# Optimization experiments

Hardware: AMD Instinct MI355X
Metric: run time of the kernel (lower is better)

Reference implementation:

```python
import jax, jax.numpy as jnp
import numpy as np

B, T, N, D = 8, 32, 24, 128          # batch, seq_len, max_node_num, roi_feature_size
H_LINK, H_LSTM, C, P = 128, 128, 6, 3  # link hidden, lstm hidden, big_attr_classes, propagate_layers


def setup_inputs() -> dict:
    key = jax.random.key(0)
    ks = jax.random.split(key, 20)
    node_num_rec = jax.random.randint(ks[0], (B, T), 2, N + 1)  # valid nodes per frame
    node_mask = jnp.arange(N)[None, None, :] < node_num_rec[:, :, None]          # [B,T,N]
    pair_mask = node_mask[:, :, :, None] & node_mask[:, :, None, :]              # [B,T,N,N]
    offdiag = ~jnp.eye(N, dtype=bool)
    # post-ResNet ROI features; invalid nodes / self-edges are zero (as in the torch code)
    node_resnet = jax.random.normal(ks[1], (B, T, D, N)) * node_mask[:, :, None, :]
    edge_resnet = jax.random.normal(ks[2], (B, T, D, N, N)) * (pair_mask & offdiag)[:, :, None]

    def w(k, shape, fan):
        return jax.random.normal(k, shape) / np.sqrt(fan)

    return dict(
        node_resnet=node_resnet, edge_resnet=edge_resnet,
        link_W1=w(ks[3], (H_LINK, D), D), link_b1=jnp.zeros((H_LINK,)),
        link_W2=w(ks[4], (1, H_LINK), H_LINK), link_b2=jnp.zeros((1,)),
        msg_Wh=w(ks[5], (D, D), 2 * D), msg_We=w(ks[6], (D, D), 2 * D), msg_b=jnp.zeros((D,)),
        gru_Wih=w(ks[7], (3 * D, D), D), gru_Whh=w(ks[8], (3 * D, D), D),
        gru_bih=jnp.zeros((3 * D,)), gru_bhh=jnp.zeros((3 * D,)),
        lstm_Wih=w(ks[9], (4 * H_LSTM, D), D), lstm_Whh=w(ks[10], (4 * H_LSTM, H_LSTM), H_LSTM),
        lstm_bih=jnp.zeros((4 * H_LSTM,)), lstm_bhh=jnp.zeros((4 * H_LSTM,)),
        ro_W=w(ks[11], (C, H_LSTM), H_LSTM), ro_b=jnp.zeros((C,)),
        node_num_rec=node_num_rec,
    )


def reference(node_resnet, edge_resnet, link_W1, link_b1, link_W2, link_b2,
              msg_Wh, msg_We, msg_b, gru_Wih, gru_Whh, gru_bih, gru_bhh,
              lstm_Wih, lstm_Whh, lstm_bih, lstm_bhh, ro_W, ro_b, node_num_rec):
    node_mask = jnp.arange(N)[None, None, :] < node_num_rec[:, :, None]      # [B,T,N]
    pair_mask = node_mask[:, :, :, None] & node_mask[:, :, None, :]          # [B,T,N,N]
    fmask_n = node_mask[:, :, None, :].astype(node_resnet.dtype)             # [B,T,1,N]
    fmask_p = pair_mask.astype(node_resnet.dtype)                            # [B,T,N,N]

    h_node = node_resnet      # [B,T,D,N]
    h_edge = edge_resnet      # [B,T,D,N,N]
    for _ in range(P):
        # link_fun (GraphConv = per-edge 1x1-conv MLP) -> adjacency logits, sigmoid gate on valid pairs
        hid = jax.nn.relu(jnp.einsum('btdvw,hd->bthvw', h_edge, link_W1)
                          + link_b1[None, None, :, None, None])
        adj = jnp.einsum('bthvw,h->btvw', hid, link_W2[0]) + link_b2[0]      # [B,T,N,N]
        gate = jax.nn.sigmoid(adj) * fmask_p
        # message_fun 'linear_concat_relu': relu(W @ concat(h_w, e_vw) + b), e_vw is raw edge feature
        msg = jax.nn.relu(jnp.einsum('btdw,od->btow', h_node, msg_Wh)[:, :, :, None, :]
                          + jnp.einsum('btdvw,od->btovw', edge_resnet, msg_We)
                          + msg_b[None, None, :, None, None])                # [B,T,D,N,N]
        gated = gate[:, :, None] * msg
        # hidden edge states of next round: gated messages in valid region, clone of edge feats elsewhere
        h_edge = jnp.where(pair_mask[:, :, None], gated, edge_resnet)
        m_v = jnp.sum(gated, axis=-1)                                        # [B,T,D,N] sum over senders
        # update_fun: single-step GRU, input m_v, hidden h_node
        x = m_v.transpose(0, 1, 3, 2)      # [B,T,N,D]
        h = h_node.transpose(0, 1, 3, 2)
        gi = x @ gru_Wih.T + gru_bih
        gh = h @ gru_Whh.T + gru_bhh
        i_r, i_z, i_n = jnp.split(gi, 3, axis=-1)
        h_r, h_z, h_n = jnp.split(gh, 3, axis=-1)
        r = jax.nn.sigmoid(i_r + h_r)
        z = jax.nn.sigmoid(i_z + h_z)
        n = jnp.tanh(i_n + r * h_n)
        h_new = ((1.0 - z) * n + z * h).transpose(0, 1, 3, 2)                # [B,T,D,N]
        h_node = jnp.where(node_mask[:, :, None, :], h_new, node_resnet)

    # temporal LSTM over seq dim; node (and batch) axis acts as LSTM batch, zero initial state
    x_seq = h_node.transpose(1, 0, 3, 2).reshape(T, B * N, D)
    h0 = jnp.zeros((B * N, H_LSTM), dtype=x_seq.dtype)
    c0 = jnp.zeros_like(h0)

    def cell(carry, xt):
        h, c = carry
        g = xt @ lstm_Wih.T + lstm_bih + h @ lstm_Whh.T + lstm_bhh
        i, f, gg, o = jnp.split(g, 4, axis=-1)
        c = jax.nn.sigmoid(f) * c + jax.nn.sigmoid(i) * jnp.tanh(gg)
        h = jax.nn.sigmoid(o) * jnp.tanh(c)
        return (h, c), h

    _, out = jax.lax.scan(cell, (h0, c0), x_seq)                             # [T,B*N,H]
    out = out.reshape(T, B, N, H_LSTM).transpose(1, 0, 2, 3)                 # [B,T,N,H]
    pred_label = (out @ ro_W.T + ro_b) * node_mask[..., None]                # [B,T,N,C]
    return pred_label
```

## Files before the change

kernel.cpp:

```cpp
#include <hip/hip_runtime.h>
#include <cmath>

typedef unsigned short u16;
typedef unsigned int   u32;
typedef short bf16x8 __attribute__((ext_vector_type(8)));
typedef float f32x4 __attribute__((ext_vector_type(4)));

constexpr int B_ = 8, T_ = 32, N_ = 24, D_ = 128;
constexpr int BT_ = B_ * T_;
constexpr int VW_ = N_ * N_;
constexpr int BTN_ = BT_ * N_;
constexpr int BTVW_ = BT_ * VW_;
constexpr int P_ = 3;
constexpr int C_ = 6;
constexpr int SA_ = 136;

__device__ __forceinline__ float bits2f(u32 u) { float f; __builtin_memcpy(&f, &u, 4); return f; }
__device__ __forceinline__ float bf2f(u16 h) { return bits2f(((u32)h) << 16); }
__device__ __forceinline__ u16 f2bf(float f) {
    u32 u; __builtin_memcpy(&u, &f, 4);
    u32 r = u + 0x7FFFu + ((u >> 16) & 1u);
    return (u16)(r >> 16);
}
__device__ __forceinline__ f32x4 ld4bf(const u16* p) {
    const uint2 v = *(const uint2*)p;
    f32x4 r;
    r[0] = bf2f((u16)v.x); r[1] = bf2f((u16)(v.x >> 16));
    r[2] = bf2f((u16)v.y); r[3] = bf2f((u16)(v.y >> 16));
    return r;
}
__device__ __forceinline__ float fexp2(float x) { return __builtin_amdgcn_exp2f(x); }
__device__ __forceinline__ float frcp(float x) { return __builtin_amdgcn_rcpf(x); }
__device__ __forceinline__ float sigm(float x) {
    return frcp(1.0f + fexp2(x * -1.4426950408889634f));
}
__device__ __forceinline__ float ftanh(float x) {
    const float t = fexp2(fabsf(x) * -2.8853900817779268f);
    return copysignf((1.0f - t) * frcp(1.0f + t), x);
}

struct PreArgs {
    const float* node; float* HN; u16* HNb;
    const float* fsrc[7]; u16* fdst[7]; int fstart[8];
    const void* csrc[10]; u16* cdst[10]; int cstart[11];
};

__global__ __launch_bounds__(256) void k_preproc(PreArgs a) {
    const int bx = blockIdx.x;
    if (bx < 256) {
        const int bt = bx;
        for (int f = threadIdx.x; f < 3072; f += 256) {
            const int d = f / 24, n = f - d * 24;
            const float v = a.node[(size_t)bt * 3072 + f];
            a.HN[(size_t)bt * 3072 + n * 128 + d] = v;
            a.HNb[(size_t)bt * 3072 + n * 128 + d] = f2bf(v);
        }
    } else if (bx < 1344) {
        const int idx = (bx - 256) * 256 + threadIdx.x;
        if (idx >= a.fstart[7]) return;
        int s = 0;
#pragma unroll
        for (int i = 1; i < 7; ++i) s += (idx >= a.fstart[i]) ? 1 : 0;
        const int off = idx - a.fstart[s];
        const int e = off & 7, lane = (off >> 3) & 63;
        const int ks = (off >> 9) & 3, rb = off >> 11;
        const int m = lane & 15, quad = lane >> 4;
        a.fdst[s][off] = f2bf(a.fsrc[s][(size_t)(rb * 16 + m) * 128 + ks * 32 + quad * 8 + e]);
    } else {
        const int idx = (bx - 1344) * 256 + threadIdx.x;
        if (idx >= a.cstart[10]) return;
        int s = 0;
#pragma unroll
        for (int i = 1; i < 10; ++i) s += (idx >= a.cstart[i]) ? 1 : 0;
        const int off = idx - a.cstart[s];
        a.cdst[s][off] = f2bf(((const float*)a.csrc[s])[off]);
    }
}

__global__ __launch_bounds__(64) void k_prep(
    const float* __restrict__ edge, const u16* __restrict__ WeF,
    const u16* __restrict__ W1F, const u16* __restrict__ b1,
    const u16* __restrict__ W2, const u16* __restrict__ b2,
    u16* __restrict__ ME, float* __restrict__ ADJ) {
    __shared__ __align__(16) u16 A[32 * 128];
    const int tid = threadIdx.x;
    const int bt = blockIdx.x / 18, tile = blockIdx.x % 18;
    const int vw0 = tile * 32;
    const size_t ebase = (size_t)bt * D_ * VW_ + vw0;
    const int vq = tid & 7, dg = tid >> 3;
    u32* A32 = (u32*)A;
#pragma unroll
    for (int batch = 0; batch < 2; ++batch) {
        float4 fa[4], fb[4];
#pragma unroll
        for (int j = 0; j < 4; ++j) {
            const int it = batch * 4 + j;
            const int d0 = it * 16 + dg * 2;
            fa[j] = *(const float4*)&edge[ebase + (size_t)d0 * VW_ + vq * 4];
            fb[j] = *(const float4*)&edge[ebase + (size_t)(d0 + 1) * VW_ + vq * 4];
        }
#pragma unroll
        for (int j = 0; j < 4; ++j) {
            const int it = batch * 4 + j;
            const int d0 = it * 16 + dg * 2;
            const float* pa = (const float*)&fa[j];
            const float* pb = (const float*)&fb[j];
#pragma unroll
            for (int i = 0; i < 4; ++i) {
                const int row = vq * 4 + i;
                const int sw32 = ((row >> 2) & 7) * 4;
                A32[row * 64 + ((d0 >> 1) ^ sw32)] =
                    (u32)f2bf(pa[i]) | ((u32)f2bf(pb[i]) << 16);
            }
        }
    }
    __syncthreads();
    const int m = tid & 15, quad = tid >> 4;
    bf16x8 a[2][4];
#pragma unroll
    for (int rt = 0; rt < 2; ++rt) {
        const int row = rt * 16 + m;
        const int sw16 = ((row >> 2) & 7) * 8;
#pragma unroll
        for (int ks = 0; ks < 4; ++ks)
            a[rt][ks] = *(const bf16x8*)&A[row * 128 + ((ks * 32 + quad * 8) ^ sw16)];
    }
    const f32x4 z = {0.f, 0.f, 0.f, 0.f};
#pragma unroll
    for (int ct = 0; ct < 8; ++ct) {
        bf16x8 bw[4];
#pragma unroll
        for (int ks = 0; ks < 4; ++ks)
            bw[ks] = *(const bf16x8*)&WeF[((ct * 4 + ks) << 9) + tid * 8];
        f32x4 acc[2];
#pragma unroll
        for (int rt = 0; rt < 2; ++rt) acc[rt] = z;
#pragma unroll
        for (int rt = 0; rt < 2; ++rt)
#pragma unroll
            for (int ks = 0; ks < 4; ++ks)
                acc[rt] = __builtin_amdgcn_mfma_f32_16x16x32_bf16(bw[ks], a[rt][ks], acc[rt], 0, 0, 0);
#pragma unroll
        for (int rt = 0; rt < 2; ++rt) {
            const u32 lo = (u32)f2bf(acc[rt][0]) | ((u32)f2bf(acc[rt][1]) << 16);
            const u32 hi = (u32)f2bf(acc[rt][2]) | ((u32)f2bf(acc[rt][3]) << 16);
            *(uint2*)&ME[(size_t)(bt * VW_ + vw0 + rt * 16 + m) * 128 + ct * 16 + quad * 4] =
                make_uint2(lo, hi);
        }
    }
    float p[2][4] = {};
    const float b2v = bf2f(b2[0]);
#pragma unroll
    for (int ct = 0; ct < 8; ++ct) {
        bf16x8 bw[4];
#pragma unroll
        for (int ks = 0; ks < 4; ++ks)
            bw[ks] = *(const bf16x8*)&W1F[((ct * 4 + ks) << 9) + tid * 8];
        f32x4 acc[2];
#pragma unroll
        for (int rt = 0; rt < 2; ++rt) acc[rt] = z;
#pragma unroll
        for (int rt = 0; rt < 2; ++rt)
#pragma unroll
            for (int ks = 0; ks < 4; ++ks)
                acc[rt] = __builtin_amdgcn_mfma_f32_16x16x32_bf16(a[rt][ks], bw[ks], acc[rt], 0, 0, 0);
        const int n = ct * 16 + m;
        const float b1v = bf2f(b1[n]);
        const float w2v = bf2f(W2[n]);
#pragma unroll
        for (int rt = 0; rt < 2; ++rt)
#pragma unroll
            for (int reg = 0; reg < 4; ++reg)
                p[rt][reg] += fmaxf(acc[rt][reg] + b1v, 0.0f) * w2v;
    }
#pragma unroll
    for (int rt = 0; rt < 2; ++rt)
#pragma unroll
        for (int reg = 0; reg < 4; ++reg) {
            float v = p[rt][reg];
            v += __shfl_xor(v, 1);
            v += __shfl_xor(v, 2);
            v += __shfl_xor(v, 4);
            v += __shfl_xor(v, 8);
            p[rt][reg] = v;
        }
    if (m == 0) {
#pragma unroll
        for (int rt = 0; rt < 2; ++rt)
#pragma unroll
            for (int reg = 0; reg < 4; ++reg)
                ADJ[bt * VW_ + vw0 + rt * 16 + quad * 4 + reg] = p[rt][reg] + b2v;
    }
}

template <bool ADJP>
__global__ __launch_bounds__(256) void k_fused(
    const u16* __restrict__ ME, const float* __restrict__ XW,
    const u16* __restrict__ mb,
    const u16* __restrict__ W1F, const u16* __restrict__ b1,
    const u16* __restrict__ W2, const u16* __restrict__ b2,
    const int* __restrict__ nnr, float* __restrict__ ADJ,
    u16* __restrict__ MVb) {
    __shared__ __align__(16) u16 A[48 * SA_];
    __shared__ float gate_s[48];
    __shared__ float2 mvp[2][2][64];
    const int tid = threadIdx.x;
    const int blk = blockIdx.x;
    const int bt = blk / 12, pr = blk - bt * 12;
    const int v0 = pr * 2;
    const int e0 = bt * VW_ + v0 * N_;
    const int nv = nnr[bt];

    if (tid < 48) gate_s[tid] = sigm(ADJ[e0 + tid]);
    __syncthreads();
    {
        const int op = tid & 63;
        const int sub = (tid >> 6) & 1;
        const int grp = tid >> 7;
        const int v = v0 + grp;
        const u32 mbu = ((const u32*)mb)[op];
        const float mb0 = bf2f((u16)mbu), mb1 = bf2f((u16)(mbu >> 16));
        const bool vva = v < nv;
        u32 meR[12]; float2 xwR[12];
#pragma unroll
        for (int i = 0; i < 12; ++i) {
            const int w = sub * 12 + i;
            const int rr = grp * 24 + w;
            meR[i] = ((const u32*)ME)[(size_t)(e0 + rr) * 64 + op];
            xwR[i] = *(const float2*)&XW[(size_t)(bt * N_ + w) * 128 + 2 * op];
        }
        float mvx = 0.0f, mvy = 0.0f;
        u32* A32 = (u32*)A;
#pragma unroll
        for (int i = 0; i < 12; ++i) {
            const int w = sub * 12 + i;
            const int rr = grp * 24 + w;
            float v0f = 0.0f, v1f = 0.0f;
            if (vva && w < nv) {
                const float g = gate_s[rr];
                v0f = g * fmaxf(xwR[i].x + bf2f((u16)meR[i]) + mb0, 0.0f);
                v1f = g * fmaxf(xwR[i].y + bf2f((u16)(meR[i] >> 16)) + mb1, 0.0f);
                mvx += v0f; mvy += v1f;
            }
            if (ADJP) A32[rr * 68 + op] = (u32)f2bf(v0f) | ((u32)f2bf(v1f) << 16);
        }
        mvp[grp][sub][op] = make_float2(mvx, mvy);
    }
    __syncthreads();
    if (tid < 128) {
        const int g2 = tid >> 6, o2 = tid & 63;
        const float2 pa = mvp[g2][0][o2], pb = mvp[g2][1][o2];
        ((u32*)MVb)[(size_t)(bt * N_ + v0 + g2) * 64 + o2] =
            (u32)f2bf(pa.x + pb.x) | ((u32)f2bf(pa.y + pb.y) << 16);
    }

    if constexpr (ADJP) {
        __syncthreads();
        if (tid >= 64) return;
        const int m = tid & 15, quad = tid >> 4;
        bf16x8 a[3][4];
#pragma unroll
        for (int rt = 0; rt < 3; ++rt)
#pragma unroll
            for (int ks = 0; ks < 4; ++ks)
                a[rt][ks] = *(const bf16x8*)&A[(rt * 16 + m) * SA_ + ks * 32 + quad * 8];
        const f32x4 z = {0.f, 0.f, 0.f, 0.f};
        float p[3][4] = {};
        const float b2v = bf2f(b2[0]);
#pragma unroll
        for (int ct = 0; ct < 8; ++ct) {
            bf16x8 bw[4];
#pragma unroll
            for (int ks = 0; ks < 4; ++ks)
                bw[ks] = *(const bf16x8*)&W1F[((ct * 4 + ks) << 9) + tid * 8];
            f32x4 acc[3];
#pragma unroll
            for (int rt = 0; rt < 3; ++rt) acc[rt] = z;
#pragma unroll
            for (int rt = 0; rt < 3; ++rt)
#pragma unroll
                for (int ks = 0; ks < 4; ++ks)
                    acc[rt] = __builtin_amdgcn_mfma_f32_16x16x32_bf16(a[rt][ks], bw[ks], acc[rt], 0, 0, 0);
            const int n = ct * 16 + m;
            const float b1v = bf2f(b1[n]);
            const float w2v = bf2f(W2[n]);
#pragma unroll
            for (int rt = 0; rt < 3; ++rt)
#pragma unroll
                for (int reg = 0; reg < 4; ++reg)
                    p[rt][reg] += fmaxf(acc[rt][reg] + b1v, 0.0f) * w2v;
        }
#pragma unroll
        for (int rt = 0; rt < 3; ++rt)
#pragma unroll
            for (int reg = 0; reg < 4; ++reg) {
                float v = p[rt][reg];
                v += __shfl_xor(v, 1);
                v += __shfl_xor(v, 2);
                v += __shfl_xor(v, 4);
                v += __shfl_xor(v, 8);
                p[rt][reg] = v;
            }
        if (m == 0) {
#pragma unroll
            for (int rt = 0; rt < 3; ++rt)
#pragma unroll
                for (int reg = 0; reg < 4; ++reg)
                    ADJ[e0 + rt * 16 + quad * 4 + reg] = p[rt][reg] + b2v;
        }
    }
}

__global__ __launch_bounds__(64, 1) void k_xw(const u16* __restrict__ HNb,
                                              const u16* __restrict__ WhF,
                                              float* __restrict__ XW) {
    const int tid = threadIdx.x;
    const int m = tid & 15, quad = tid >> 4;
    const int r0 = blockIdx.x * 16;
    const int ct0 = blockIdx.y * 2;
    bf16x8 a[4];
#pragma unroll
    for (int ks = 0; ks < 4; ++ks)
        a[ks] = *(const bf16x8*)&HNb[(size_t)(r0 + m) * 128 + ks * 32 + quad * 8];
    const f32x4 z = {0.f, 0.f, 0.f, 0.f};
#pragma unroll
    for (int cti = 0; cti < 2; ++cti) {
        const int ct = ct0 + cti;
        f32x4 acc = z;
#pragma unroll
        for (int ks = 0; ks < 4; ++ks) {
            const bf16x8 b = *(const bf16x8*)&WhF[((ct * 4 + ks) << 9) + tid * 8];
            acc = __builtin_amdgcn_mfma_f32_16x16x32_bf16(b, a[ks], acc, 0, 0, 0);
        }
        *(f32x4*)&XW[(size_t)(r0 + m) * 128 + ct * 16 + quad * 4] = acc;
    }
}

__global__ __launch_bounds__(64, 1) void k_gruM(
    const u16* __restrict__ MVb, const u16* __restrict__ HNb_in,
    float* __restrict__ HN, u16* __restrict__ HNb,
    const u16* __restrict__ WihF, const u16* __restrict__ WhhF,
    const u16* __restrict__ bih, const u16* __restrict__ bhh,
    const int* __restrict__ nnr) {
    const int tid = threadIdx.x;
    const int m = tid & 15, quad = tid >> 4;
    const int rbase = blockIdx.x * 16;
    const int ct0 = blockIdx.y * 2;
    bf16x8 amv[4], ahn[4];
#pragma unroll
    for (int ks = 0; ks < 4; ++ks) {
        amv[ks] = *(const bf16x8*)&MVb[(size_t)(rbase + m) * 128 + ks * 32 + quad * 8];
        ahn[ks] = *(const bf16x8*)&HNb_in[(size_t)(rbase + m) * 128 + ks * 32 + quad * 8];
    }
    const int myrow = rbase + m;
    const int mybt = myrow / N_;
    const bool valid = (myrow - mybt * N_) < nnr[mybt];
    const f32x4 z = {0.f, 0.f, 0.f, 0.f};
#pragma unroll
    for (int cti = 0; cti < 2; ++cti) {
        const int ct = ct0 + cti;
        f32x4 gi[3], gh[3];
#pragma unroll
        for (int g = 0; g < 3; ++g) { gi[g] = z; gh[g] = z; }
#pragma unroll
        for (int g = 0; g < 3; ++g) {
            const int rb = g * 8 + ct;
#pragma unroll
            for (int ks = 0; ks < 4; ++ks) {
                const bf16x8 bi_f = *(const bf16x8*)&WihF[((rb * 4 + ks) << 9) + tid * 8];
                const bf16x8 bh_f = *(const bf16x8*)&WhhF[((rb * 4 + ks) << 9) + tid * 8];
                gi[g] = __builtin_amdgcn_mfma_f32_16x16x32_bf16(bi_f, amv[ks], gi[g], 0, 0, 0);
                gh[g] = __builtin_amdgcn_mfma_f32_16x16x32_bf16(bh_f, ahn[ks], gh[g], 0, 0, 0);
            }
        }
        const int col0 = ct * 16 + quad * 4;
        const f32x4 biR = ld4bf(&bih[col0]),       bhR = ld4bf(&bhh[col0]);
        const f32x4 biZ = ld4bf(&bih[128 + col0]), bhZ = ld4bf(&bhh[128 + col0]);
        const f32x4 biN = ld4bf(&bih[256 + col0]), bhN = ld4bf(&bhh[256 + col0]);
        const size_t oi = (size_t)myrow * 128 + col0;
        const f32x4 hold = *(const f32x4*)&HN[oi];
        f32x4 hv;
#pragma unroll
        for (int reg = 0; reg < 4; ++reg) {
            const float r  = sigm(gi[0][reg] + gh[0][reg] + biR[reg] + bhR[reg]);
            const float zz = sigm(gi[1][reg] + gh[1][reg] + biZ[reg] + bhZ[reg]);
            const float nn = ftanh(gi[2][reg] + biN[reg] + r * (gh[2][reg] + bhN[reg]));
            hv[reg] = valid ? ((1.0f - zz) * nn + zz * hold[reg]) : 0.0f;
        }
        *(f32x4*)&HN[oi] = hv;
        const u32 lo = (u32)f2bf(hv[0]) | ((u32)f2bf(hv[1]) << 16);
        const u32 hi = (u32)f2bf(hv[2]) | ((u32)f2bf(hv[3]) << 16);
        *(uint2*)&HNb[oi] = make_uint2(lo, hi);
    }
}

__global__ __launch_bounds__(64, 2) void k_gi(const u16* __restrict__ HNb,
                                              const u16* __restrict__ WF,
                                              const u16* __restrict__ bih, const u16* __restrict__ bhh,
                                              float* __restrict__ GI2) {
    const int tid = threadIdx.x;
    const int m = tid & 15, quad = tid >> 4;
    const int r0 = blockIdx.x * 16;
    const int ocol0 = blockIdx.y * 64;
    const int r = r0 + m;
    const int btq = r / 24, n = r - btq * 24;
    const int b = btq >> 5, t = btq & 31;
    const int q = b * 24 + n;
    const int blk = q >> 4, mrow = q & 15;
    bf16x8 a[4];
#pragma unroll
    for (int ks = 0; ks < 4; ++ks)
        a[ks] = *(const bf16x8*)&HNb[(size_t)r * 128 + ks * 32 + quad * 8];
    const f32x4 z = {0.f, 0.f, 0.f, 0.f};
#pragma unroll
    for (int ct = 0; ct < 4; ++ct) {
        f32x4 acc = z;
        const int rb = blockIdx.y * 4 + ct;
#pragma unroll
        for (int ks = 0; ks < 4; ++ks) {
            const bf16x8 bb = *(const bf16x8*)&WF[((rb * 4 + ks) << 9) + tid * 8];
            acc = __builtin_amdgcn_mfma_f32_16x16x32_bf16(bb, a[ks], acc, 0, 0, 0);
        }
        const int col0 = ocol0 + ct * 16 + quad * 4;
        const f32x4 bi4 = ld4bf(&bih[col0]);
        const f32x4 bh4 = ld4bf(&bhh[col0]);
#pragma unroll
        for (int reg = 0; reg < 4; ++reg) acc[reg] += bi4[reg] + bh4[reg];
        const int cta = (ocol0 >> 4) + ct;
        const int w = cta & 7, j = cta >> 3;
        const size_t addr = ((size_t)(blk * 32 + t) * 512 + (w * 64 + quad * 16 + mrow)) * 16 + j * 4;
        *(f32x4*)&GI2[addr] = acc;
    }
}

__global__ __launch_bounds__(512) void k_rec(const float* __restrict__ GI2,
                                             const u16* __restrict__ WhhF,
                                             float* __restrict__ OUTH) {
    __shared__ __align__(16) u16 Abuf[2][16 * 128];
    const int tid = threadIdx.x;
    const int w = tid >> 6, lane = tid & 63;
    const int m = lane & 15, quad = lane >> 4;
    const int blk = blockIdx.x;
    const int q = blk * 16 + m;
    bf16x8 bw[4][4];
#pragma unroll
    for (int j = 0; j < 4; ++j)
#pragma unroll
        for (int ks = 0; ks < 4; ++ks)
            bw[j][ks] = *(const bf16x8*)&WhhF[(((j * 8 + w) * 4 + ks) << 9) + lane * 8];
    const f32x4 z = {0.f, 0.f, 0.f, 0.f};
    f32x4 cst = z;
    bf16x8 a[4];
#pragma unroll
    for (int ks = 0; ks < 4; ++ks) a[ks] = (bf16x8)(short)0;
    const float* gb = GI2 + ((size_t)blk * 32 * 512 + tid) * 16;
    f32x4 g[4], gn[4];
#pragma unroll
    for (int j = 0; j < 4; ++j) g[j] = *(const f32x4*)&gb[j * 4];
    const int ws = w * 2 + (quad >> 1);
    const int woff = (quad & 1) * 2;
    for (int t = 0; t < T_; ++t) {
        const int tn = (t + 1 < T_) ? (t + 1) : (T_ - 1);
        const size_t gnb = (size_t)tn * 512 * 16;
#pragma unroll
        for (int j = 0; j < 4; ++j) gn[j] = *(const f32x4*)&gb[gnb + j * 4];
        f32x4 acc[4];
#pragma unroll
        for (int j = 0; j < 4; ++j) acc[j] = z;
#pragma unroll
        for (int j = 0; j < 4; ++j)
#pragma unroll
            for (int ks = 0; ks < 4; ++ks)
                acc[j] = __builtin_amdgcn_mfma_f32_16x16x32_bf16(bw[j][ks], a[ks], acc[j], 0, 0, 0);
        f32x4 hv;
#pragma unroll
        for (int r = 0; r < 4; ++r) {
            const float gi_ = acc[0][r] + g[0][r];
            const float gf_ = acc[1][r] + g[1][r];
            const float gg_ = acc[2][r] + g[2][r];
            const float go_ = acc[3][r] + g[3][r];
            cst[r] = sigm(gf_) * cst[r] + sigm(gi_) * ftanh(gg_);
            hv[r] = sigm(go_) * ftanh(cst[r]);
        }
        *(f32x4*)&OUTH[((size_t)t * 192 + q) * 128 + w * 16 + quad * 4] = hv;
        const u32 lo = (u32)f2bf(hv[0]) | ((u32)f2bf(hv[1]) << 16);
        const u32 hi = (u32)f2bf(hv[2]) | ((u32)f2bf(hv[3]) << 16);
        u32* dst = (u32*)&Abuf[(t + 1) & 1][0];
        *(uint2*)&dst[m * 64 + ((ws ^ m) << 2) + woff] = make_uint2(lo, hi);
        __syncthreads();
        const u16* src = &Abuf[(t + 1) & 1][0];
#pragma unroll
        for (int ks = 0; ks < 4; ++ks)
            a[ks] = *(const bf16x8*)&src[m * 128 + (((ks * 4 + quad) ^ m) << 3)];
#pragma unroll
        for (int j = 0; j < 4; ++j) g[j] = gn[j];
    }
}

__global__ __launch_bounds__(256) void k_readout(const float* __restrict__ OUTH,
                                                 const u16* __restrict__ roW,
                                                 const u16* __restrict__ rob,
                                                 const int* __restrict__ nnr,
                                                 float* __restrict__ out) {
    const int idx = blockIdx.x * 256 + threadIdx.x;
    const int btn = idx / C_, c = idx - btn * C_;
    const int bt = btn / N_, n = btn - bt * N_;
    const int b = bt / T_, t = bt - b * T_;
    const int nv = nnr[bt];
    float val = 0.0f;
    if (n < nv) {
        const float* hrow = OUTH + ((size_t)t * 192 + b * N_ + n) * 128;
        const uint2* w2 = (const uint2*)&roW[c * 128];
        float acc = bf2f(rob[c]);
#pragma unroll
        for (int k4 = 0; k4 < 32; ++k4) {
            const float4 h4 = *(const float4*)&hrow[k4 * 4];
            const uint2 ww = w2[k4];
            acc = fmaf(bf2f((u16)ww.x), h4.x,
                  fmaf(bf2f((u16)(ww.x >> 16)), h4.y,
                  fmaf(bf2f((u16)ww.y), h4.z,
                  fmaf(bf2f((u16)(ww.y >> 16)), h4.w, acc))));
        }
        val = acc;
    }
    out[idx] = val;
}

extern "C" void kernel_launch(void* const* d_in, const int* in_sizes, int n_in,
                              void* d_out, int out_size, void* d_ws, size_t ws_size,
                              hipStream_t stream) {
    const float* node = (const float*)d_in[0];
    const float* edge = (const float*)d_in[1];
    const int* nnr = (const int*)d_in[19];

    char* ws = (char*)d_ws;
    float* HN = (float*)ws;   ws += (size_t)BTN_ * D_ * 4;
    u16* HNb = (u16*)ws;      ws += (size_t)BTN_ * D_ * 2;
    float* XW = (float*)ws;   ws += (size_t)BTN_ * D_ * 4;
    u16* MVb = (u16*)ws;      ws += (size_t)BTN_ * D_ * 2;
    float* ADJ = (float*)ws;  ws += (size_t)BTVW_ * 4;
    float* GI = (float*)ws;   ws += (size_t)BTN_ * 512 * 4;
    u16* WThh = (u16*)ws;     ws += 65536 * 2;
    u16* ME = (u16*)ws;       ws += (size_t)BTVW_ * D_ * 2;
    float* OUTH = XW;

    u16* cbase = (u16*)ws;
    const int cvtN17[17] = {16384, 128, 128, 1, 16384, 16384, 128,
                            49152, 49152, 384, 384, 65536, 65536, 512, 512, 768, 6};
    u16* cptr[17];
    {
        int off = 0;
        for (int i = 0; i < 17; ++i) {
            cptr[i] = cbase + off;
            off += (cvtN17[i] + 7) & ~7;
        }
    }
    PreArgs pa;
    pa.node = node; pa.HN = HN; pa.HNb = HNb;
    {
        const int din_idx[7] = {2, 6, 7, 9, 10, 13, 14};
        const int slot[7]    = {0, 4, 5, 7,  8, 11, 12};
        const int nelem[7]   = {16384, 16384, 16384, 49152, 49152, 65536, 65536};
        int cum = 0;
        for (int i = 0; i < 7; ++i) {
            pa.fsrc[i] = (const float*)d_in[din_idx[i]];
            pa.fdst[i] = cptr[slot[i]];
            pa.fstart[i] = cum;
            cum += nelem[i];
        }
        pa.fstart[7] = cum;
    }
    {
        const int din_idx[10] = {3, 4, 5, 8, 11, 12, 15, 16, 17, 18};
        const int slot[10]    = {1, 2, 3, 6,  9, 10, 13, 14, 15, 16};
        const int nelem[10]   = {128, 128, 1, 128, 384, 384, 512, 512, 768, 6};
        int cum = 0;
        for (int i = 0; i < 10; ++i) {
            pa.csrc[i] = d_in[din_idx[i]];
            pa.cdst[i] = cptr[slot[i]];
            pa.cstart[i] = cum;
            cum += nelem[i];
        }
        pa.cstart[10] = cum;
    }
    u16* fW1 = cptr[0];  u16* cb1 = cptr[1];  u16* cW2 = cptr[2];  u16* cb2 = cptr[3];
    u16* fWh = cptr[4];  u16* fWe = cptr[5];  u16* cmb = cptr[6];
    u16* fgWih = cptr[7]; u16* fgWhh = cptr[8]; u16* cgbih = cptr[9]; u16* cgbhh = cptr[10];
    u16* flsWih = cptr[11]; u16* flsWhh = cptr[12]; u16* clsbih = cptr[13]; u16* clsbhh = cptr[14];
    u16* croW = cptr[15]; u16* crob = cptr[16];
    (void)WThh;

    k_preproc<<<1356, 256, 0, stream>>>(pa);
    k_prep<<<BT_ * 18, 64, 0, stream>>>(edge, fWe, fW1, cb1, cW2, cb2, ME, ADJ);
    for (int l = 0; l < P_; ++l) {
        k_xw<<<dim3(384, 4), 64, 0, stream>>>(HNb, fWh, XW);
        if (l < P_ - 1)
            k_fused<true><<<BTN_ / 2, 256, 0, stream>>>(ME, XW, cmb, fW1, cb1, cW2, cb2,
                                                        nnr, ADJ, MVb);
        else
            k_fused<false><<<BTN_ / 2, 256, 0, stream>>>(ME, XW, cmb, fW1, cb1, cW2, cb2,
                                                         nnr, ADJ, MVb);
        k_gruM<<<dim3(384, 4), 64, 0, stream>>>(MVb, HNb, HN, HNb, fgWih, fgWhh, cgbih, cgbhh, nnr);
    }
    k_gi<<<dim3(384, 8), 64, 0, stream>>>(HNb, flsWih, clsbih, clsbhh, GI);
    k_rec<<<12, 512, 0, stream>>>(GI, flsWhh, OUTH);
    k_readout<<<144, 256, 0, stream>>>(OUTH, croW, crob, nnr, (float*)d_out);
}
```

Before: 317.7 us.

## Fuse node-hidden projection into message kernel and split prep across two waves

The separate k_xw launch is removed. Each k_fused block now computes its frame's 24x128 hidden-state projection with MFMA into shared memory, so the fp32 XW buffer no longer makes a round trip through global memory. That projection is recomputed redundantly in all 12 blocks per frame. Separately, k_prep now runs with 128 threads, and the edge-message GEMM and the link-score GEMM are split across two wavefronts so they run in parallel.

```diff
diff --git a/kernel.cpp b/kernel.cpp
--- a/kernel.cpp
+++ b/kernel.cpp
@@ -77,7 +77,7 @@
     }
 }
 
-__global__ __launch_bounds__(64) void k_prep(
+__global__ __launch_bounds__(128) void k_prep(
     const float* __restrict__ edge, const u16* __restrict__ WeF,
     const u16* __restrict__ W1F, const u16* __restrict__ b1,
     const u16* __restrict__ W2, const u16* __restrict__ b2,
@@ -89,22 +89,19 @@
     const size_t ebase = (size_t)bt * D_ * VW_ + vw0;
     const int vq = tid & 7, dg = tid >> 3;
     u32* A32 = (u32*)A;
-#pragma unroll
-    for (int batch = 0; batch < 2; ++batch) {
+    {
         float4 fa[4], fb[4];
 #pragma unroll
-        for (int j = 0; j < 4; ++j) {
-            const int it = batch * 4 + j;
-            const int d0 = it * 16 + dg * 2;
-            fa[j] = *(const float4*)&edge[ebase + (size_t)d0 * VW_ + vq * 4];
-            fb[j] = *(const float4*)&edge[ebase + (size_t)(d0 + 1) * VW_ + vq * 4];
-        }
-#pragma unroll
-        for (int j = 0; j < 4; ++j) {
-            const int it = batch * 4 + j;
-            const int d0 = it * 16 + dg * 2;
-            const float* pa = (const float*)&fa[j];
-            const float* pb = (const float*)&fb[j];
+        for (int it = 0; it < 4; ++it) {
+            const int d0 = it * 32 + dg * 2;
+            fa[it] = *(const float4*)&edge[ebase + (size_t)d0 * VW_ + vq * 4];
+            fb[it] = *(const float4*)&edge[ebase + (size_t)(d0 + 1) * VW_ + vq * 4];
+        }
+#pragma unroll
+        for (int it = 0; it < 4; ++it) {
+            const int d0 = it * 32 + dg * 2;
+            const float* pa = (const float*)&fa[it];
+            const float* pb = (const float*)&fb[it];
 #pragma unroll
             for (int i = 0; i < 4; ++i) {
                 const int row = vq * 4 + i;
@@ -115,7 +112,8 @@
         }
     }
     __syncthreads();
-    const int m = tid & 15, quad = tid >> 4;
+    const int wv = tid >> 6, lane = tid & 63;
+    const int m = lane & 15, quad = lane >> 4;
     bf16x8 a[2][4];
 #pragma unroll
     for (int rt = 0; rt < 2; ++rt) {
@@ -126,77 +124,80 @@
             a[rt][ks] = *(const bf16x8*)&A[row * 128 + ((ks * 32 + quad * 8) ^ sw16)];
     }
     const f32x4 z = {0.f, 0.f, 0.f, 0.f};
-#pragma unroll
-    for (int ct = 0; ct < 8; ++ct) {
-        bf16x8 bw[4];
-#pragma unroll
-        for (int ks = 0; ks < 4; ++ks)
-            bw[ks] = *(const bf16x8*)&WeF[((ct * 4 + ks) << 9) + tid * 8];
-        f32x4 acc[2];
-#pragma unroll
-        for (int rt = 0; rt < 2; ++rt) acc[rt] = z;
+    if (wv == 0) {
+#pragma unroll
+        for (int ct = 0; ct < 8; ++ct) {
+            bf16x8 bw[4];
+#pragma unroll
+            for (int ks = 0; ks < 4; ++ks)
+                bw[ks] = *(const bf16x8*)&WeF[((ct * 4 + ks) << 9) + lane * 8];
+            f32x4 acc[2];
+#pragma unroll
+            for (int rt = 0; rt < 2; ++rt) acc[rt] = z;
+#pragma unroll
+            for (int rt = 0; rt < 2; ++rt)
+#pragma unroll
+                for (int ks = 0; ks < 4; ++ks)
+                    acc[rt] = __builtin_amdgcn_mfma_f32_16x16x32_bf16(bw[ks], a[rt][ks], acc[rt], 0, 0, 0);
+#pragma unroll
+            for (int rt = 0; rt < 2; ++rt) {
+                const u32 lo = (u32)f2bf(acc[rt][0]) | ((u32)f2bf(acc[rt][1]) << 16);
+                const u32 hi = (u32)f2bf(acc[rt][2]) | ((u32)f2bf(acc[rt][3]) << 16);
+                *(uint2*)&ME[(size_t)(bt * VW_ + vw0 + rt * 16 + m) * 128 + ct * 16 + quad * 4] =
+                    make_uint2(lo, hi);
+            }
+        }
+    } else {
+        float p[2][4] = {};
+        const float b2v = bf2f(b2[0]);
+#pragma unroll
+        for (int ct = 0; ct < 8; ++ct) {
+            bf16x8 bw[4];
+#pragma unroll
+            for (int ks = 0; ks < 4; ++ks)
+                bw[ks] = *(const bf16x8*)&W1F[((ct * 4 + ks) << 9) + lane * 8];
+            f32x4 acc[2];
+#pragma unroll
+            for (int rt = 0; rt < 2; ++rt) acc[rt] = z;
+#pragma unroll
+            for (int rt = 0; rt < 2; ++rt)
+#pragma unroll
+                for (int ks = 0; ks < 4; ++ks)
+                    acc[rt] = __builtin_amdgcn_mfma_f32_16x16x32_bf16(a[rt][ks], bw[ks], acc[rt], 0, 0, 0);
+            const int n = ct * 16 + m;
+            const float b1v = bf2f(b1[n]);
+            const float w2v = bf2f(W2[n]);
+#pragma unroll
+            for (int rt = 0; rt < 2; ++rt)
+#pragma unroll
+                for (int reg = 0; reg < 4; ++reg)
+                    p[rt][reg] += fmaxf(acc[rt][reg] + b1v, 0.0f) * w2v;
+        }
 #pragma unroll
         for (int rt = 0; rt < 2; ++rt)
 #pragma unroll
-            for (int ks = 0; ks < 4; ++ks)
-                acc[rt] = __builtin_amdgcn_mfma_f32_16x16x32_bf16(bw[ks], a[rt][ks], acc[rt], 0, 0, 0);
-#pragma unroll
-        for (int rt = 0; rt < 2; ++rt) {
-            const u32 lo = (u32)f2bf(acc[rt][0]) | ((u32)f2bf(acc[rt][1]) << 16);
-            const u32 hi = (u32)f2bf(acc[rt][2]) | ((u32)f2bf(acc[rt][3]) << 16);
-            *(uint2*)&ME[(size_t)(bt * VW_ + vw0 + rt * 16 + m) * 128 + ct * 16 + quad * 4] =
-                make_uint2(lo, hi);
-        }
-    }
-    float p[2][4] = {};
-    const float b2v = bf2f(b2[0]);
-#pragma unroll
-    for (int ct = 0; ct < 8; ++ct) {
-        bf16x8 bw[4];
-#pragma unroll
-        for (int ks = 0; ks < 4; ++ks)
-            bw[ks] = *(const bf16x8*)&W1F[((ct * 4 + ks) << 9) + tid * 8];
-        f32x4 acc[2];
-#pragma unroll
-        for (int rt = 0; rt < 2; ++rt) acc[rt] = z;
-#pragma unroll
-        for (int rt = 0; rt < 2; ++rt)
-#pragma unroll
-            for (int ks = 0; ks < 4; ++ks)
-                acc[rt] = __builtin_amdgcn_mfma_f32_16x16x32_bf16(a[rt][ks], bw[ks], acc[rt], 0, 0, 0);
-        const int n = ct * 16 + m;
-        const float b1v = bf2f(b1[n]);
-        const float w2v = bf2f(W2[n]);
-#pragma unroll
-        for (int rt = 0; rt < 2; ++rt)
-#pragma unroll
-            for (int reg = 0; reg < 4; ++reg)
-                p[rt][reg] += fmaxf(acc[rt][reg] + b1v, 0.0f) * w2v;
-    }
-#pragma unroll
-    for (int rt = 0; rt < 2; ++rt)
-#pragma unroll
-        for (int reg = 0; reg < 4; ++reg) {
-            float v = p[rt][reg];
-            v += __shfl_xor(v, 1);
-            v += __shfl_xor(v, 2);
-            v += __shfl_xor(v, 4);
-            v += __shfl_xor(v, 8);
-            p[rt][reg] = v;
-        }
-    if (m == 0) {
-#pragma unroll
-        for (int rt = 0; rt < 2; ++rt)
-#pragma unroll
-            for (int reg = 0; reg < 4; ++reg)
-                ADJ[bt * VW_ + vw0 + rt * 16 + quad * 4 + reg] = p[rt][reg] + b2v;
+            for (int reg = 0; reg < 4; ++reg) {
+                float v = p[rt][reg];
+                v += __shfl_xor(v, 1);
+                v += __shfl_xor(v, 2);
+                v += __shfl_xor(v, 4);
+                v += __shfl_xor(v, 8);
+                p[rt][reg] = v;
+            }
+        if (m == 0) {
+#pragma unroll
+            for (int rt = 0; rt < 2; ++rt)
+#pragma unroll
+                for (int reg = 0; reg < 4; ++reg)
+                    ADJ[bt * VW_ + vw0 + rt * 16 + quad * 4 + reg] = p[rt][reg] + b2v;
+        }
     }
 }
 
 template <bool ADJP>
 __global__ __launch_bounds__(256) void k_fused(
-    const u16* __restrict__ ME, const float* __restrict__ XW,
-    const u16* __restrict__ mb,
+    const u16* __restrict__ ME, const u16* __restrict__ HNb,
+    const u16* __restrict__ WhF, const u16* __restrict__ mb,
     const u16* __restrict__ W1F, const u16* __restrict__ b1,
     const u16* __restrict__ W2, const u16* __restrict__ b2,
     const int* __restrict__ nnr, float* __restrict__ ADJ,
@@ -204,6 +205,7 @@
     __shared__ __align__(16) u16 A[48 * SA_];
     __shared__ float gate_s[48];
     __shared__ float2 mvp[2][2][64];
+    __shared__ __align__(16) float XWs[24][132];
     const int tid = threadIdx.x;
     const int blk = blockIdx.x;
     const int bt = blk / 12, pr = blk - bt * 12;
@@ -212,6 +214,30 @@
     const int nv = nnr[bt];
 
     if (tid < 48) gate_s[tid] = sigm(ADJ[e0 + tid]);
+    {
+        const int wv = tid >> 6, lane = tid & 63;
+        if (wv < 2) {
+            const int m = lane & 15, quad = lane >> 4;
+            int rr = bt * 24 + wv * 16 + m;
+            if (rr > BTN_ - 1) rr = BTN_ - 1;
+            bf16x8 ah[4];
+#pragma unroll
+            for (int ks = 0; ks < 4; ++ks)
+                ah[ks] = *(const bf16x8*)&HNb[(size_t)rr * 128 + ks * 32 + quad * 8];
+            const f32x4 z = {0.f, 0.f, 0.f, 0.f};
+            const int lrow = wv * 16 + m;
+#pragma unroll
+            for (int ct = 0; ct < 8; ++ct) {
+                f32x4 acc = z;
+#pragma unroll
+                for (int ks = 0; ks < 4; ++ks) {
+                    const bf16x8 b = *(const bf16x8*)&WhF[((ct * 4 + ks) << 9) + lane * 8];
+                    acc = __builtin_amdgcn_mfma_f32_16x16x32_bf16(b, ah[ks], acc, 0, 0, 0);
+                }
+                if (lrow < 24) *(f32x4*)&XWs[lrow][ct * 16 + quad * 4] = acc;
+            }
+        }
+    }
     __syncthreads();
     {
         const int op = tid & 63;
@@ -221,13 +247,12 @@
         const u32 mbu = ((const u32*)mb)[op];
         const float mb0 = bf2f((u16)mbu), mb1 = bf2f((u16)(mbu >> 16));
         const bool vva = v < nv;
-        u32 meR[12]; float2 xwR[12];
+        u32 meR[12];
 #pragma unroll
         for (int i = 0; i < 12; ++i) {
             const int w = sub * 12 + i;
             const int rr = grp * 24 + w;
             meR[i] = ((const u32*)ME)[(size_t)(e0 + rr) * 64 + op];
-            xwR[i] = *(const float2*)&XW[(size_t)(bt * N_ + w) * 128 + 2 * op];
         }
         float mvx = 0.0f, mvy = 0.0f;
         u32* A32 = (u32*)A;
@@ -238,8 +263,9 @@
             float v0f = 0.0f, v1f = 0.0f;
             if (vva && w < nv) {
                 const float g = gate_s[rr];
-                v0f = g * fmaxf(xwR[i].x + bf2f((u16)meR[i]) + mb0, 0.0f);
-                v1f = g * fmaxf(xwR[i].y + bf2f((u16)(meR[i] >> 16)) + mb1, 0.0f);
+                const float2 xw = *(const float2*)&XWs[w][2 * op];
+                v0f = g * fmaxf(xw.x + bf2f((u16)meR[i]) + mb0, 0.0f);
+                v1f = g * fmaxf(xw.y + bf2f((u16)(meR[i] >> 16)) + mb1, 0.0f);
                 mvx += v0f; mvy += v1f;
             }
             if (ADJP) A32[rr * 68 + op] = (u32)f2bf(v0f) | ((u32)f2bf(v1f) << 16);
@@ -308,31 +334,6 @@
                 for (int reg = 0; reg < 4; ++reg)
                     ADJ[e0 + rt * 16 + quad * 4 + reg] = p[rt][reg] + b2v;
         }
-    }
-}
-
-__global__ __launch_bounds__(64, 1) void k_xw(const u16* __restrict__ HNb,
-                                              const u16* __restrict__ WhF,
-                                              float* __restrict__ XW) {
-    const int tid = threadIdx.x;
-    const int m = tid & 15, quad = tid >> 4;
-    const int r0 = blockIdx.x * 16;
-    const int ct0 = blockIdx.y * 2;
-    bf16x8 a[4];
-#pragma unroll
-    for (int ks = 0; ks < 4; ++ks)
-        a[ks] = *(const bf16x8*)&HNb[(size_t)(r0 + m) * 128 + ks * 32 + quad * 8];
-    const f32x4 z = {0.f, 0.f, 0.f, 0.f};
-#pragma unroll
-    for (int cti = 0; cti < 2; ++cti) {
-        const int ct = ct0 + cti;
-        f32x4 acc = z;
-#pragma unroll
-        for (int ks = 0; ks < 4; ++ks) {
-            const bf16x8 b = *(const bf16x8*)&WhF[((ct * 4 + ks) << 9) + tid * 8];
-            acc = __builtin_amdgcn_mfma_f32_16x16x32_bf16(b, a[ks], acc, 0, 0, 0);
-        }
-        *(f32x4*)&XW[(size_t)(r0 + m) * 128 + ct * 16 + quad * 4] = acc;
     }
 }
 
@@ -591,14 +592,13 @@
     (void)WThh;
 
     k_preproc<<<1356, 256, 0, stream>>>(pa);
-    k_prep<<<BT_ * 18, 64, 0, stream>>>(edge, fWe, fW1, cb1, cW2, cb2, ME, ADJ);
+    k_prep<<<BT_ * 18, 128, 0, stream>>>(edge, fWe, fW1, cb1, cW2, cb2, ME, ADJ);
     for (int l = 0; l < P_; ++l) {
-        k_xw<<<dim3(384, 4), 64, 0, stream>>>(HNb, fWh, XW);
         if (l < P_ - 1)
-            k_fused<true><<<BTN_ / 2, 256, 0, stream>>>(ME, XW, cmb, fW1, cb1, cW2, cb2,
+            k_fused<true><<<BTN_ / 2, 256, 0, stream>>>(ME, HNb, fWh, cmb, fW1, cb1, cW2, cb2,
                                                         nnr, ADJ, MVb);
         else
-            k_fused<false><<<BTN_ / 2, 256, 0, stream>>>(ME, XW, cmb, fW1, cb1, cW2, cb2,
+            k_fused<false><<<BTN_ / 2, 256, 0, stream>>>(ME, HNb, fWh, cmb, fW1, cb1, cW2, cb2,
                                                          nnr, ADJ, MVb);
         k_gruM<<<dim3(384, 4), 64, 0, stream>>>(MVb, HNb, HN, HNb, fgWih, fgWhh, cgbih, cgbhh, nnr);
     }
```

New measurement: 324.8 us. 1.02x slower.
